# Performance work log

Hardware: AMD Instinct MI355X
Metric: run time of the kernel (lower is better)

Reference implementation:

```python
import math
import jax, jax.numpy as jnp
import numpy as np

B, C, H, W = 32, 256, 32, 32  # in==mid==out channels

def setup_inputs() -> dict:
    key = jax.random.key(0)
    ks = jax.random.split(key, 3)
    x = jax.random.normal(ks[0], (B, C, H, W), dtype=jnp.float32)
    # 1x1 convs are just channel matmuls: weight [out_ch, in_ch]
    w_in = jax.random.normal(ks[1], (3 * C, C), dtype=jnp.float32) * (1.0 / math.sqrt(C))
    b_in = jnp.zeros((3 * C,), dtype=jnp.float32)
    # project_out has init_scale=0.0 in the original; we use random weights so the
    # output (and gradients) are non-trivial, but the math is identical.
    w_out = jax.random.normal(ks[2], (C, C), dtype=jnp.float32) * (1.0 / math.sqrt(C))
    b_out = jnp.zeros((C,), dtype=jnp.float32)
    return {"x": x, "w_in": w_in, "b_in": b_in, "w_out": w_out, "b_out": b_out}

def _qkv_attention(q, k, v):
    # q,k,v: [B,C,H,W]. Full spatial self-attention over the HxW grid.
    b, c, h, w = q.shape
    scores = jnp.einsum('bchw,bcHW->bhwHW', q, k)          # [B,H,W,H,W]
    scores = scores.reshape(b, h, w, h * w) / math.sqrt(c)
    attn = jax.nn.softmax(scores, axis=-1).reshape(b, h, w, h, w)
    return jnp.einsum('bhwHW,bcHW->bchw', attn, v)          # [B,C,H,W]

def reference(x, w_in, b_in, w_out, b_out):
    skip = x  # in_channels == out_channels -> Identity skip
    qkv = jnp.einsum('oc,bchw->bohw', w_in, x) + b_in[None, :, None, None]
    q, k, v = jnp.split(qkv, 3, axis=1)
    h = _qkv_attention(q, k, v)
    out = jnp.einsum('oc,bchw->bohw', w_out, h) + b_out[None, :, None, None]
    return out + skip
```

## Files before the change

kernel.cpp:

```cpp
#include <hip/hip_runtime.h>
#include <hip/hip_bf16.h>

typedef __attribute__((ext_vector_type(8))) short bf16x8;
typedef __attribute__((ext_vector_type(4))) float f32x4;
typedef __attribute__((ext_vector_type(16))) float f32x16;
typedef long long i64;

#define NB 32
#define NC 256
#define NN 1024

__device__ __forceinline__ unsigned pack2(float a, float b) {
    __hip_bfloat16 ha = __float2bfloat16(a), hb = __float2bfloat16(b);
    unsigned short ua = *(unsigned short*)&ha, ub = *(unsigned short*)&hb;
    return (unsigned)ua | ((unsigned)ub << 16);
}

__device__ __forceinline__ float bflo(unsigned u) {
    union { unsigned i; float f; } x; x.i = u << 16; return x.f;
}
__device__ __forceinline__ float bfhi(unsigned u) {
    union { unsigned i; float f; } x; x.i = u & 0xffff0000u; return x.f;
}
__device__ __forceinline__ unsigned fp8x4(float a, float b, float c, float d) {
    int w = __builtin_amdgcn_cvt_pk_fp8_f32(a, b, 0, false);
    w = __builtin_amdgcn_cvt_pk_fp8_f32(c, d, w, true);
    return (unsigned)w;
}

__device__ __forceinline__ void glds16(const void* g, void* lds) {
    __builtin_amdgcn_global_load_lds(
        (const __attribute__((address_space(1))) unsigned int*)g,
        (__attribute__((address_space(3))) unsigned int*)lds, 16, 0, 0);
}

__global__ __launch_bounds__(256) void xpose_kernel(
    const float* __restrict__ x, __hip_bfloat16* __restrict__ Xt)
{
    __shared__ float Ls[64 * 67];
    const int t = threadIdx.x;
    const int n0 = blockIdx.x * 64, c0 = blockIdx.y * 64, b = blockIdx.z;
    const int cl = t >> 4, nl = (t & 15) * 4;
    const float* xb = x + ((size_t)b * NC + c0) * NN + n0;
    #pragma unroll
    for (int q4 = 0; q4 < 4; ++q4) {
        const int c = cl + q4 * 16;
        const float4 v = *(const float4*)(xb + (size_t)c * NN + nl);
        Ls[(nl + 0) * 67 + c] = v.x;
        Ls[(nl + 1) * 67 + c] = v.y;
        Ls[(nl + 2) * 67 + c] = v.z;
        Ls[(nl + 3) * 67 + c] = v.w;
    }
    __syncthreads();
    #pragma unroll
    for (int p = 0; p < 2; ++p) {
        const int idx = p * 256 + t, n = idx >> 3, cs = idx & 7;
        const float* r = &Ls[n * 67 + cs * 8];
        uint4 o;
        o.x = pack2(r[0], r[1]); o.y = pack2(r[2], r[3]);
        o.z = pack2(r[4], r[5]); o.w = pack2(r[6], r[7]);
        *(uint4*)(Xt + ((size_t)b * NN + n0 + n) * NC + c0 + cs * 8) = o;
    }
}

__device__ __forceinline__ void stage_ab(const __hip_bfloat16* __restrict__ Ag,
                                         const float* __restrict__ Bg,
                                         char* Ad, char* Bd, int ks, int t)
{
    const int srow = t >> 3, spch = t & 7;
    #pragma unroll
    for (int it = 0; it < 4; ++it) {
        const int row = it * 32 + srow;
        const int sw  = row & 7;
        glds16(Ag + (size_t)row * NC + ks * 64 + ((spch ^ sw) << 3),
               Ad + (it * 256 + t) * 16);
        const float* wp = Bg + (size_t)row * NC + ks * 64 + (spch << 3);
        const float4 u0 = *(const float4*)wp;
        const float4 u1 = *(const float4*)(wp + 4);
        uint4 pk;
        pk.x = pack2(u0.x, u0.y); pk.y = pack2(u0.z, u0.w);
        pk.z = pack2(u1.x, u1.y); pk.w = pack2(u1.z, u1.w);
        *(uint4*)(Bd + row * 128 + ((spch ^ sw) << 4)) = pk;
    }
}

__global__ __launch_bounds__(256, 2) void qkv_gemm_kernel(
    const __hip_bfloat16* __restrict__ Xt, const float* __restrict__ w_in,
    const float* __restrict__ b_in, unsigned char* __restrict__ Qt8,
    unsigned char* __restrict__ Kt8, unsigned char* __restrict__ Vf8)
{
    __shared__ char smem[65536];
    char* const A0 = smem;
    char* const A1 = smem + 16384;
    char* const B0 = smem + 32768;
    char* const B1 = smem + 49152;

    const int t  = threadIdx.x;
    const int wv = t >> 6, ln = t & 63, lo = ln & 15, hi = ln >> 4;
    const int wm = wv >> 1, wn = wv & 1;
    const int n0 = blockIdx.x * 128, o0 = blockIdx.y * 128, b = blockIdx.z;

    const __hip_bfloat16* Ag = Xt + ((size_t)b * NN + n0) * NC;
    const float* Bg = w_in + (size_t)o0 * NC;

    f32x4 acc[4][4];
    #pragma unroll
    for (int i = 0; i < 4; ++i)
        #pragma unroll
        for (int j = 0; j < 4; ++j) acc[i][j] = (f32x4){0.f, 0.f, 0.f, 0.f};

    int ra[4], rb[4];
    #pragma unroll
    for (int f = 0; f < 4; ++f) { ra[f] = wm * 64 + f * 16 + lo; rb[f] = wn * 64 + f * 16 + lo; }

    stage_ab(Ag, Bg, A0, B0, 0, t);
    __syncthreads();
    #pragma unroll
    for (int ks = 0; ks < 4; ++ks) {
        char* Ac = (ks & 1) ? A1 : A0;
        char* Bc = (ks & 1) ? B1 : B0;
        if (ks < 3)
            stage_ab(Ag, Bg, (ks & 1) ? A0 : A1, (ks & 1) ? B0 : B1, ks + 1, t);
        #pragma unroll
        for (int kk = 0; kk < 2; ++kk) {
            bf16x8 av[4], bv[4];
            #pragma unroll
            for (int f = 0; f < 4; ++f) {
                av[f] = *(const bf16x8*)(Ac + ra[f] * 128 + (((kk << 2) | hi) ^ (ra[f] & 7)) * 16);
                bv[f] = *(const bf16x8*)(Bc + rb[f] * 128 + (((kk << 2) | hi) ^ (rb[f] & 7)) * 16);
            }
            #pragma unroll
            for (int fm = 0; fm < 4; ++fm)
                #pragma unroll
                for (int fn = 0; fn < 4; ++fn)
                    acc[fm][fn] = __builtin_amdgcn_mfma_f32_16x16x32_bf16(
                        av[fm], bv[fn], acc[fm][fn], 0, 0, 0);
        }
        __syncthreads();
    }

    float bias[4];
    #pragma unroll
    for (int fn = 0; fn < 4; ++fn) bias[fn] = b_in[o0 + wn * 64 + fn * 16 + lo];

    __hip_bfloat16* Ls = (__hip_bfloat16*)smem;
    if (o0 < 512) {
        #pragma unroll
        for (int fm = 0; fm < 4; ++fm)
            #pragma unroll
            for (int fn = 0; fn < 4; ++fn)
                #pragma unroll
                for (int r = 0; r < 4; ++r)
                    Ls[(wm * 64 + fm * 16 + hi * 4 + r) * 136 + wn * 64 + fn * 16 + lo] =
                        __float2bfloat16(acc[fm][fn][r] + bias[fn]);
        __syncthreads();
        unsigned char* dst = (o0 < 256) ? Qt8 : Kt8;
        const int oc = (o0 < 256) ? o0 : o0 - 256;
        #pragma unroll
        for (int p = 0; p < 4; ++p) {
            const int idx = p * 256 + t, row = idx >> 3, ch = idx & 7;
            const unsigned* ls = (const unsigned*)&Ls[row * 136 + ch * 16];
            const uint4 a = *(const uint4*)ls;
            const uint4 b2 = *(const uint4*)(ls + 4);
            uint4 o;
            o.x = fp8x4(bflo(a.x), bfhi(a.x), bflo(a.y), bfhi(a.y));
            o.y = fp8x4(bflo(a.z), bfhi(a.z), bflo(a.w), bfhi(a.w));
            o.z = fp8x4(bflo(b2.x), bfhi(b2.x), bflo(b2.y), bfhi(b2.y));
            o.w = fp8x4(bflo(b2.z), bfhi(b2.z), bflo(b2.w), bfhi(b2.w));
            *(uint4*)(dst + ((size_t)b * NN + n0 + row) * 256 + oc + ch * 16) = o;
        }
    } else {
        #pragma unroll
        for (int fm = 0; fm < 4; ++fm)
            #pragma unroll
            for (int fn = 0; fn < 4; ++fn)
                #pragma unroll
                for (int r = 0; r < 4; ++r)
                    Ls[(wn * 64 + fn * 16 + lo) * 136 + wm * 64 + fm * 16 + hi * 4 + r] =
                        __float2bfloat16(acc[fm][fn][r] + bias[fn]);
        __syncthreads();
        #pragma unroll
        for (int p = 0; p < 8; ++p) {
            const int idx = p * 256 + t;
            const int ch = idx >> 7, cr = idx & 127;
            const unsigned* ls = (const unsigned*)&Ls[cr * 136 + ch * 8];
            const uint4 a = *(const uint4*)ls;
            uint2 o;
            o.x = fp8x4(bflo(a.x), bfhi(a.x), bflo(a.y), bfhi(a.y));
            o.y = fp8x4(bflo(a.z), bfhi(a.z), bflo(a.w), bfhi(a.w));
            const int g = (n0 >> 3) + ch;
            *(uint2*)(Vf8 + (((size_t)b * 128 + g) * 256 + (o0 - 512) + cr) * 8) = o;
        }
    }
}

__device__ __forceinline__ void stage_tile(const unsigned char* __restrict__ Kb,
                                           const unsigned char* __restrict__ Vb,
                                           char* Kd, char* Vd, int m0, int t)
{
    {
        const int row = t >> 4, pc = t & 15;
        const int prow = (row & 19) | ((row & 4) << 1) | ((row & 8) >> 1);
        const int sc = pc ^ (row & 15);
        glds16(Kb + (size_t)(m0 + prow) * 256 + sc * 16, Kd + t * 16);
    }
    {
        glds16(Vb + (size_t)(m0 >> 3) * 2048 + t * 16, Vd + t * 16);
    }
}

__global__ __launch_bounds__(512, 2) void attn_kernel(
    const unsigned char* __restrict__ Qt8, const unsigned char* __restrict__ Kt8,
    const unsigned char* __restrict__ Vf8, __hip_bfloat16* __restrict__ Ht)
{
    __shared__ char smem[139264];

    const int t  = threadIdx.x;
    const int wv = t >> 6, ln = t & 63;
    const int l32 = ln & 31, h2 = ln >> 5;
    const int qgrp = wv & 3, half = wv >> 2;
    const int wid = blockIdx.x + 8 * blockIdx.y;
    const int swz = (wid & 7) * 32 + (wid >> 3);
    const int qb = swz & 7, b = swz >> 3;
    const int n0 = qb * 128;
    const float scale = 0.0625f;

    const unsigned char* Kbase = Kt8 + (size_t)b * NN * 256;
    const unsigned char* Vbase = Vf8 + (size_t)b * 128 * 2048;

    const unsigned char* qp = Qt8 + ((size_t)b * NN + n0 + qgrp * 32 + l32) * 256;
    i64 qf[16];
    #pragma unroll
    for (int ks = 0; ks < 16; ++ks)
        qf[ks] = *(const i64*)(qp + ks * 16 + h2 * 8);

    f32x16 acc[8];
    #pragma unroll
    for (int ct = 0; ct < 8; ++ct)
        #pragma unroll
        for (int r = 0; r < 16; ++r) acc[ct][r] = 0.f;
    float mr = 0.f;
    float sr = 0.f;

    #pragma unroll
    for (int tt = 0; tt < 4; ++tt)
        stage_tile(Kbase, Vbase, smem + tt * 8192, smem + 32768 + tt * 8192,
                   tt * 32, t);
    __syncthreads();

    for (int s = 0; s < 16; ++s) {
        if (s < 15) {
            const int t2 = 2 * s + 2, t3 = 2 * s + 3;
            stage_tile(Kbase, Vbase, smem + (t2 & 3) * 8192,
                       smem + 32768 + (t2 & 3) * 8192, t2 * 32, t);
            stage_tile(Kbase, Vbase, smem + (t3 & 3) * 8192,
                       smem + 32768 + (t3 & 3) * 8192, t3 * 32, t);
        }
        const int tile = 2 * s + half;
        char* const Kc = smem + (tile & 3) * 8192;
        char* const Vc = smem + 32768 + (tile & 3) * 8192;

        f32x16 sfA, sfB;
        #pragma unroll
        for (int r = 0; r < 16; ++r) { sfA[r] = 0.f; sfB[r] = 0.f; }
        __builtin_amdgcn_s_setprio(1);
        #pragma unroll
        for (int ks = 0; ks < 8; ++ks) {
            const int pc = ks ^ (l32 & 15);
            const i64 kf = *(const i64*)(Kc + l32 * 256 + pc * 16 + h2 * 8);
            sfA = __builtin_amdgcn_mfma_f32_32x32x16_fp8_fp8(kf, qf[ks], sfA, 0, 0, 0);
        }
        #pragma unroll
        for (int ks = 8; ks < 16; ++ks) {
            const int pc = ks ^ (l32 & 15);
            const i64 kf = *(const i64*)(Kc + l32 * 256 + pc * 16 + h2 * 8);
            sfB = __builtin_amdgcn_mfma_f32_32x32x16_fp8_fp8(kf, qf[ks], sfB, 0, 0, 0);
        }
        __builtin_amdgcn_s_setprio(0);

        float sv[16];
        #pragma unroll
        for (int r = 0; r < 16; ++r) sv[r] = sfA[r] + sfB[r];

        float m0a = fmaxf(sv[0], sv[1]),  m1a = fmaxf(sv[2], sv[3]);
        float m2a = fmaxf(sv[4], sv[5]),  m3a = fmaxf(sv[6], sv[7]);
        float m4a = fmaxf(sv[8], sv[9]),  m5a = fmaxf(sv[10], sv[11]);
        float m6a = fmaxf(sv[12], sv[13]), m7a = fmaxf(sv[14], sv[15]);
        float m0b = fmaxf(m0a, m1a), m1b = fmaxf(m2a, m3a);
        float m2b = fmaxf(m4a, m5a), m3b = fmaxf(m6a, m7a);
        float tm = fmaxf(fmaxf(m0b, m1b), fmaxf(m2b, m3b));
        tm = fmaxf(tm, __shfl_xor(tm, 32, 64));
        tm *= scale;
        if (__any(tm > mr + 8.f)) {
            const float mn = fmaxf(mr, tm);
            const float al = __expf(mr - mn);
            mr = mn;
            sr *= al;
            #pragma unroll
            for (int ct = 0; ct < 8; ++ct)
                #pragma unroll
                for (int r = 0; r < 16; ++r) acc[ct][r] *= al;
        }
        float p[16];
        #pragma unroll
        for (int r = 0; r < 16; ++r)
            p[r] = __expf(sv[r] * scale - mr);
        float s0a = p[0] + p[1],  s1a = p[2] + p[3];
        float s2a = p[4] + p[5],  s3a = p[6] + p[7];
        float s4a = p[8] + p[9],  s5a = p[10] + p[11];
        float s6a = p[12] + p[13], s7a = p[14] + p[15];
        float sacc = ((s0a + s1a) + (s2a + s3a)) + ((s4a + s5a) + (s6a + s7a));
        sacc += __shfl_xor(sacc, 32, 64);
        sr += sacc;

        i64 pb[2];
        #pragma unroll
        for (int kstep = 0; kstep < 2; ++kstep) {
            union { unsigned u[2]; i64 l; } uu;
            uu.u[0] = fp8x4(p[8 * kstep + 0], p[8 * kstep + 1],
                            p[8 * kstep + 2], p[8 * kstep + 3]);
            uu.u[1] = fp8x4(p[8 * kstep + 4], p[8 * kstep + 5],
                            p[8 * kstep + 6], p[8 * kstep + 7]);
            pb[kstep] = uu.l;
        }

        __builtin_amdgcn_s_setprio(1);
        #pragma unroll
        for (int ct = 0; ct < 8; ++ct) {
            #pragma unroll
            for (int kstep = 0; kstep < 2; ++kstep) {
                const i64 vf = *(const i64*)(Vc + (2 * kstep + h2) * 2048 +
                                             (ct * 32 + l32) * 8);
                acc[ct] = __builtin_amdgcn_mfma_f32_32x32x16_fp8_fp8(vf, pb[kstep], acc[ct], 0, 0, 0);
            }
        }
        __builtin_amdgcn_s_setprio(0);
        __syncthreads();
    }

    float* const ex = (float*)smem;
    const int slot = (qgrp * 64 + ln) * 136;
    if (half) {
        float* dst = ex + slot;
        #pragma unroll
        for (int ct = 0; ct < 8; ++ct)
            #pragma unroll
            for (int rr = 0; rr < 4; ++rr) {
                f32x4 v = {acc[ct][rr * 4 + 0], acc[ct][rr * 4 + 1],
                           acc[ct][rr * 4 + 2], acc[ct][rr * 4 + 3]};
                *(f32x4*)(dst + ct * 16 + rr * 4) = v;
            }
        dst[128] = mr;
        dst[129] = sr;
    }
    __syncthreads();
    if (!half) {
        const float* src = ex + slot;
        const float mb = src[128], lb = src[129];
        const float m = fmaxf(mr, mb);
        float fa = __expf(mr - m), fb = __expf(mb - m);
        const float inv = 1.0f / (sr * fa + lb * fb);
        fa *= inv; fb *= inv;
        __hip_bfloat16* hp = Ht + ((size_t)b * NN + n0 + qgrp * 32 + l32) * NC;
        #pragma unroll
        for (int ct = 0; ct < 8; ++ct)
            #pragma unroll
            for (int ss = 0; ss < 4; ++ss) {
                const float o0 = acc[ct][ss * 4 + 0] * fa + src[ct * 16 + ss * 4 + 0] * fb;
                const float o1 = acc[ct][ss * 4 + 1] * fa + src[ct * 16 + ss * 4 + 1] * fb;
                const float o2 = acc[ct][ss * 4 + 2] * fa + src[ct * 16 + ss * 4 + 2] * fb;
                const float o3 = acc[ct][ss * 4 + 3] * fa + src[ct * 16 + ss * 4 + 3] * fb;
                uint2 v;
                v.x = pack2(o0, o1);
                v.y = pack2(o2, o3);
                *(uint2*)(hp + ct * 32 + ss * 8 + h2 * 4) = v;
            }
    }
}

__global__ __launch_bounds__(256, 2) void out_gemm_kernel(
    const __hip_bfloat16* __restrict__ Ht, const float* __restrict__ w_out,
    const float* __restrict__ b_out, const float* __restrict__ x,
    float* __restrict__ out)
{
    __shared__ char smem[65536];
    char* const A0 = smem;
    char* const A1 = smem + 16384;
    char* const B0 = smem + 32768;
    char* const B1 = smem + 49152;

    const int t  = threadIdx.x;
    const int wv = t >> 6, ln = t & 63, lo = ln & 15, hi = ln >> 4;
    const int wm = wv >> 1, wn = wv & 1;
    const int n0 = blockIdx.x * 128, o0 = blockIdx.y * 128, b = blockIdx.z;

    const float* Ag = w_out + (size_t)o0 * NC;
    const __hip_bfloat16* Bg = Ht + ((size_t)b * NN + n0) * NC;

    f32x4 acc[4][4];
    #pragma unroll
    for (int i = 0; i < 4; ++i)
        #pragma unroll
        for (int j = 0; j < 4; ++j) acc[i][j] = (f32x4){0.f, 0.f, 0.f, 0.f};

    int ra[4], rb[4];
    #pragma unroll
    for (int f = 0; f < 4; ++f) { ra[f] = wm * 64 + f * 16 + lo; rb[f] = wn * 64 + f * 16 + lo; }

    stage_ab(Bg, Ag, B0, A0, 0, t);
    __syncthreads();
    #pragma unroll
    for (int ks = 0; ks < 4; ++ks) {
        char* Ac = (ks & 1) ? A1 : A0;
        char* Bc = (ks & 1) ? B1 : B0;
        if (ks < 3)
            stage_ab(Bg, Ag, (ks & 1) ? B0 : B1, (ks & 1) ? A0 : A1, ks + 1, t);
        #pragma unroll
        for (int kk = 0; kk < 2; ++kk) {
            bf16x8 av[4], bv[4];
            #pragma unroll
            for (int f = 0; f < 4; ++f) {
                av[f] = *(const bf16x8*)(Ac + ra[f] * 128 + (((kk << 2) | hi) ^ (ra[f] & 7)) * 16);
                bv[f] = *(const bf16x8*)(Bc + rb[f] * 128 + (((kk << 2) | hi) ^ (rb[f] & 7)) * 16);
            }
            #pragma unroll
            for (int fm = 0; fm < 4; ++fm)
                #pragma unroll
                for (int fn = 0; fn < 4; ++fn)
                    acc[fm][fn] = __builtin_amdgcn_mfma_f32_16x16x32_bf16(
                        av[fm], bv[fn], acc[fm][fn], 0, 0, 0);
        }
        __syncthreads();
    }

    #pragma unroll
    for (int fm = 0; fm < 4; ++fm) {
        #pragma unroll
        for (int r = 0; r < 4; ++r) {
            const int o = o0 + wm * 64 + fm * 16 + hi * 4 + r;
            const float bo = b_out[o];
            const size_t rowg = ((size_t)b * NC + o) * NN + n0;
            #pragma unroll
            for (int fn = 0; fn < 4; ++fn) {
                const size_t gi = rowg + wn * 64 + fn * 16 + lo;
                out[gi] = acc[fm][fn][r] + bo + x[gi];
            }
        }
    }
}

extern "C" void kernel_launch(void* const* d_in, const int* in_sizes, int n_in,
                              void* d_out, int out_size, void* d_ws, size_t ws_size,
                              hipStream_t stream) {
    const float* x     = (const float*)d_in[0];
    const float* w_in  = (const float*)d_in[1];
    const float* b_in  = (const float*)d_in[2];
    const float* w_out = (const float*)d_in[3];
    const float* b_out = (const float*)d_in[4];
    float* out = (float*)d_out;

    if (ws_size < (size_t)64 * 1024 * 1024) return;
    char* ws = (char*)d_ws;
    unsigned char* Qt8 = (unsigned char*)(ws);
    unsigned char* Kt8 = (unsigned char*)(ws + ((size_t)8 << 20));
    unsigned char* Vf8 = (unsigned char*)(ws + ((size_t)16 << 20));
    __hip_bfloat16* Ht = (__hip_bfloat16*)(ws + ((size_t)32 << 20));
    __hip_bfloat16* Xt = (__hip_bfloat16*)(ws + ((size_t)48 << 20));

    xpose_kernel<<<dim3(16, 4, 32), 256, 0, stream>>>(x, Xt);
    qkv_gemm_kernel<<<dim3(8, 6, 32), 256, 0, stream>>>(Xt, w_in, b_in, Qt8, Kt8, Vf8);
    attn_kernel<<<dim3(8, 32), 512, 0, stream>>>(Qt8, Kt8, Vf8, Ht);
    out_gemm_kernel<<<dim3(8, 2, 32), 256, 0, stream>>>(Ht, w_out, b_out, x, out);
}
```

Measured before the change: 92.65 us.

## Fuse output projection GEMM into attention kernel epilogue

Removes the separate out_gemm kernel. The attention kernel now merges its two half-results into a bf16 H tile held in shared memory, converts w_out to bf16 in LDS in two 128-row halves, and runs the projection with 32x32 MFMAs before adding bias and the residual. This drops the global round trip of H and one kernel launch. In exchange, every attention block redundantly reconverts the full w_out, the tail of the attention kernel becomes longer and more serialized, and only 256 blocks now do the projection work.

```diff
diff --git a/kernel.cpp b/kernel.cpp
--- a/kernel.cpp
+++ b/kernel.cpp
@@ -211,7 +211,9 @@
 
 __global__ __launch_bounds__(512, 2) void attn_kernel(
     const unsigned char* __restrict__ Qt8, const unsigned char* __restrict__ Kt8,
-    const unsigned char* __restrict__ Vf8, __hip_bfloat16* __restrict__ Ht)
+    const unsigned char* __restrict__ Vf8, const float* __restrict__ w_out,
+    const float* __restrict__ b_out, const float* __restrict__ xg,
+    float* __restrict__ out)
 {
     __shared__ char smem[139264];
 
@@ -339,113 +341,92 @@
     }
 
     float* const ex = (float*)smem;
-    const int slot = (qgrp * 64 + ln) * 136;
-    if (half) {
-        float* dst = ex + slot;
-        #pragma unroll
-        for (int ct = 0; ct < 8; ++ct)
-            #pragma unroll
-            for (int rr = 0; rr < 4; ++rr) {
-                f32x4 v = {acc[ct][rr * 4 + 0], acc[ct][rr * 4 + 1],
-                           acc[ct][rr * 4 + 2], acc[ct][rr * 4 + 3]};
-                *(f32x4*)(dst + ct * 16 + rr * 4) = v;
-            }
-        dst[128] = mr;
-        dst[129] = sr;
-    }
-    __syncthreads();
-    if (!half) {
-        const float* src = ex + slot;
-        const float mb = src[128], lb = src[129];
-        const float m = fmaxf(mr, mb);
-        float fa = __expf(mr - m), fb = __expf(mb - m);
-        const float inv = 1.0f / (sr * fa + lb * fb);
-        fa *= inv; fb *= inv;
-        __hip_bfloat16* hp = Ht + ((size_t)b * NN + n0 + qgrp * 32 + l32) * NC;
-        #pragma unroll
-        for (int ct = 0; ct < 8; ++ct)
-            #pragma unroll
-            for (int ss = 0; ss < 4; ++ss) {
-                const float o0 = acc[ct][ss * 4 + 0] * fa + src[ct * 16 + ss * 4 + 0] * fb;
-                const float o1 = acc[ct][ss * 4 + 1] * fa + src[ct * 16 + ss * 4 + 1] * fb;
-                const float o2 = acc[ct][ss * 4 + 2] * fa + src[ct * 16 + ss * 4 + 2] * fb;
-                const float o3 = acc[ct][ss * 4 + 3] * fa + src[ct * 16 + ss * 4 + 3] * fb;
-                uint2 v;
-                v.x = pack2(o0, o1);
-                v.y = pack2(o2, o3);
-                *(uint2*)(hp + ct * 32 + ss * 8 + h2 * 4) = v;
-            }
-    }
-}
-
-__global__ __launch_bounds__(256, 2) void out_gemm_kernel(
-    const __hip_bfloat16* __restrict__ Ht, const float* __restrict__ w_out,
-    const float* __restrict__ b_out, const float* __restrict__ x,
-    float* __restrict__ out)
-{
-    __shared__ char smem[65536];
-    char* const A0 = smem;
-    char* const A1 = smem + 16384;
-    char* const B0 = smem + 32768;
-    char* const B1 = smem + 49152;
-
-    const int t  = threadIdx.x;
-    const int wv = t >> 6, ln = t & 63, lo = ln & 15, hi = ln >> 4;
-    const int wm = wv >> 1, wn = wv & 1;
-    const int n0 = blockIdx.x * 128, o0 = blockIdx.y * 128, b = blockIdx.z;
-
-    const float* Ag = w_out + (size_t)o0 * NC;
-    const __hip_bfloat16* Bg = Ht + ((size_t)b * NN + n0) * NC;
-
-    f32x4 acc[4][4];
-    #pragma unroll
-    for (int i = 0; i < 4; ++i)
-        #pragma unroll
-        for (int j = 0; j < 4; ++j) acc[i][j] = (f32x4){0.f, 0.f, 0.f, 0.f};
-
-    int ra[4], rb[4];
-    #pragma unroll
-    for (int f = 0; f < 4; ++f) { ra[f] = wm * 64 + f * 16 + lo; rb[f] = wn * 64 + f * 16 + lo; }
-
-    stage_ab(Bg, Ag, B0, A0, 0, t);
-    __syncthreads();
-    #pragma unroll
-    for (int ks = 0; ks < 4; ++ks) {
-        char* Ac = (ks & 1) ? A1 : A0;
-        char* Bc = (ks & 1) ? B1 : B0;
-        if (ks < 3)
-            stage_ab(Bg, Ag, (ks & 1) ? B0 : B1, (ks & 1) ? A0 : A1, ks + 1, t);
-        #pragma unroll
-        for (int kk = 0; kk < 2; ++kk) {
-            bf16x8 av[4], bv[4];
-            #pragma unroll
-            for (int f = 0; f < 4; ++f) {
-                av[f] = *(const bf16x8*)(Ac + ra[f] * 128 + (((kk << 2) | hi) ^ (ra[f] & 7)) * 16);
-                bv[f] = *(const bf16x8*)(Bc + rb[f] * 128 + (((kk << 2) | hi) ^ (rb[f] & 7)) * 16);
-            }
-            #pragma unroll
-            for (int fm = 0; fm < 4; ++fm)
-                #pragma unroll
-                for (int fn = 0; fn < 4; ++fn)
-                    acc[fm][fn] = __builtin_amdgcn_mfma_f32_16x16x32_bf16(
-                        av[fm], bv[fn], acc[fm][fn], 0, 0, 0);
-        }
-        __syncthreads();
-    }
-
-    #pragma unroll
-    for (int fm = 0; fm < 4; ++fm) {
-        #pragma unroll
-        for (int r = 0; r < 4; ++r) {
-            const int o = o0 + wm * 64 + fm * 16 + hi * 4 + r;
+    __hip_bfloat16* const Hld = (__hip_bfloat16*)(smem + 69632);
+    #pragma unroll
+    for (int ph = 0; ph < 2; ++ph) {
+        if (half == 1 && (qgrp >> 1) == ph) {
+            float* dst = ex + ((qgrp & 1) * 64 + ln) * 132;
+            #pragma unroll
+            for (int ct = 0; ct < 8; ++ct)
+                #pragma unroll
+                for (int rr = 0; rr < 4; ++rr) {
+                    f32x4 v = {acc[ct][rr * 4 + 0], acc[ct][rr * 4 + 1],
+                               acc[ct][rr * 4 + 2], acc[ct][rr * 4 + 3]};
+                    *(f32x4*)(dst + ct * 16 + rr * 4) = v;
+                }
+            dst[128] = mr;
+            dst[129] = sr;
+        }
+        __syncthreads();
+        if (half == 0 && (qgrp >> 1) == ph) {
+            const float* src = ex + ((qgrp & 1) * 64 + ln) * 132;
+            const float mb = src[128], lb = src[129];
+            const float m = fmaxf(mr, mb);
+            float fa = __expf(mr - m), fb = __expf(mb - m);
+            const float inv = 1.0f / (sr * fa + lb * fb);
+            fa *= inv; fb *= inv;
+            __hip_bfloat16* hrow = Hld + (size_t)(qgrp * 32 + l32) * 264;
+            #pragma unroll
+            for (int ct = 0; ct < 8; ++ct)
+                #pragma unroll
+                for (int ss = 0; ss < 4; ++ss) {
+                    const float o0 = acc[ct][ss * 4 + 0] * fa + src[ct * 16 + ss * 4 + 0] * fb;
+                    const float o1 = acc[ct][ss * 4 + 1] * fa + src[ct * 16 + ss * 4 + 1] * fb;
+                    const float o2 = acc[ct][ss * 4 + 2] * fa + src[ct * 16 + ss * 4 + 2] * fb;
+                    const float o3 = acc[ct][ss * 4 + 3] * fa + src[ct * 16 + ss * 4 + 3] * fb;
+                    uint2 v;
+                    v.x = pack2(o0, o1);
+                    v.y = pack2(o2, o3);
+                    *(uint2*)(hrow + ct * 32 + ss * 8 + h2 * 4) = v;
+                }
+        }
+        __syncthreads();
+    }
+
+    __hip_bfloat16* const Wld = (__hip_bfloat16*)smem;
+    const int oT = wv >> 1;
+    const int nT0 = (wv & 1) * 2, nT1 = nT0 + 1;
+    for (int oh = 0; oh < 2; ++oh) {
+        #pragma unroll
+        for (int p = 0; p < 8; ++p) {
+            const int idx = p * 512 + t;
+            const int o = idx >> 5, ck = idx & 31;
+            const float* wp = w_out + (size_t)(oh * 128 + o) * NC + ck * 8;
+            const float4 u0 = *(const float4*)wp;
+            const float4 u1 = *(const float4*)(wp + 4);
+            uint4 pk;
+            pk.x = pack2(u0.x, u0.y); pk.y = pack2(u0.z, u0.w);
+            pk.z = pack2(u1.x, u1.y); pk.w = pack2(u1.z, u1.w);
+            *(uint4*)((char*)Wld + (size_t)o * 528 + ck * 16) = pk;
+        }
+        __syncthreads();
+
+        f32x16 oc0, oc1;
+        #pragma unroll
+        for (int r = 0; r < 16; ++r) { oc0[r] = 0.f; oc1[r] = 0.f; }
+        __builtin_amdgcn_s_setprio(1);
+        #pragma unroll
+        for (int ks = 0; ks < 16; ++ks) {
+            const int ck = ks * 2 + h2;
+            bf16x8 wf = *(const bf16x8*)((char*)Wld + (size_t)(oT * 32 + l32) * 528 + ck * 16);
+            bf16x8 hf0 = *(const bf16x8*)((char*)Hld + (size_t)(nT0 * 32 + l32) * 528 + ck * 16);
+            bf16x8 hf1 = *(const bf16x8*)((char*)Hld + (size_t)(nT1 * 32 + l32) * 528 + ck * 16);
+            oc0 = __builtin_amdgcn_mfma_f32_32x32x16_bf16(wf, hf0, oc0, 0, 0, 0);
+            oc1 = __builtin_amdgcn_mfma_f32_32x32x16_bf16(wf, hf1, oc1, 0, 0, 0);
+        }
+        __builtin_amdgcn_s_setprio(0);
+
+        #pragma unroll
+        for (int r = 0; r < 16; ++r) {
+            const int o = oh * 128 + oT * 32 + (r & 3) + 8 * (r >> 2) + 4 * h2;
             const float bo = b_out[o];
             const size_t rowg = ((size_t)b * NC + o) * NN + n0;
-            #pragma unroll
-            for (int fn = 0; fn < 4; ++fn) {
-                const size_t gi = rowg + wn * 64 + fn * 16 + lo;
-                out[gi] = acc[fm][fn][r] + bo + x[gi];
-            }
-        }
+            const size_t g0 = rowg + nT0 * 32 + l32;
+            const size_t g1 = rowg + nT1 * 32 + l32;
+            out[g0] = oc0[r] + bo + xg[g0];
+            out[g1] = oc1[r] + bo + xg[g1];
+        }
+        __syncthreads();
     }
 }
 
@@ -464,11 +445,9 @@
     unsigned char* Qt8 = (unsigned char*)(ws);
     unsigned char* Kt8 = (unsigned char*)(ws + ((size_t)8 << 20));
     unsigned char* Vf8 = (unsigned char*)(ws + ((size_t)16 << 20));
-    __hip_bfloat16* Ht = (__hip_bfloat16*)(ws + ((size_t)32 << 20));
-    __hip_bfloat16* Xt = (__hip_bfloat16*)(ws + ((size_t)48 << 20));
+    __hip_bfloat16* Xt = (__hip_bfloat16*)(ws + ((size_t)24 << 20));
 
     xpose_kernel<<<dim3(16, 4, 32), 256, 0, stream>>>(x, Xt);
     qkv_gemm_kernel<<<dim3(8, 6, 32), 256, 0, stream>>>(Xt, w_in, b_in, Qt8, Kt8, Vf8);
-    attn_kernel<<<dim3(8, 32), 512, 0, stream>>>(Qt8, Kt8, Vf8, Ht);
-    out_gemm_kernel<<<dim3(8, 2, 32), 256, 0, stream>>>(Ht, w_out, b_out, x, out);
-}
+    attn_kernel<<<dim3(8, 32), 512, 0, stream>>>(Qt8, Kt8, Vf8, w_out, b_out, x, out);
+}
```

After: 88.03 us. 5.0% less time.
